# Optimization experiments

Hardware: AMD Instinct MI355X
Metric: run time of the kernel (lower is better)

## Reference

```python
import jax, jax.numpy as jnp
import numpy as np

DN = ('NCHW', 'OIHW', 'NCHW')
NUM_DOMAINS = 4


def conv2d(x, w, pad, groups=1):
    return jax.lax.conv_general_dilated(x, w, (1, 1), pad, dimension_numbers=DN,
                                        feature_group_count=groups)


def batchnorm2d(x, w, b, eps=1e-3):
    m = x.mean(axis=(0, 2, 3), keepdims=True)
    v = x.var(axis=(0, 2, 3), keepdims=True)
    return (x - m) / jnp.sqrt(v + eps) * w[None, :, None, None] + b[None, :, None, None]


def avgpool_w(x, k):
    B, C, H, W = x.shape
    Wo = W // k
    return x[..., :Wo * k].reshape(B, C, H, Wo, k).mean(axis=-1)


def mink(u, v):
    # Minkowski inner product <u,v>_L = -u0*v0 + <us,vs>
    return -u[..., 0] * v[..., 0] + (u[..., 1:] * v[..., 1:]).sum(-1)


def lorentz_elu(x):
    s = jax.nn.elu(x[..., 1:])
    t = jnp.sqrt(1.0 + (s * s).sum(-1, keepdims=True))
    return jnp.concatenate([t, s], -1)


def lorentz_avgpool_w(x, k):
    # (B,H,W,C) Lorentz points; window mean then Lorentz centroid projection
    B, H, W, C = x.shape
    Wo = W // k
    s = x[:, :, :Wo * k].reshape(B, H, Wo, k, C).mean(axis=3)
    d = jnp.sqrt(jnp.clip(jnp.abs(mink(s, s)), 1e-8, None))[..., None]
    return s / d


def lorentz_dbn(x, domains, beta, gamma, eps=1e-5):
    # Domain-specific Riemannian batch norm on the Lorentz manifold (k=1),
    # scalar dispersion (Frechet-mean centroid + geodesic variance per domain).
    B, H, W, C = x.shape
    pts = x.reshape(B, H * W, C)
    npts = float(H * W)
    s = jax.ops.segment_sum(pts.sum(axis=1), domains, num_segments=NUM_DOMAINS)  # (D,C)
    cnt = jax.ops.segment_sum(jnp.full((B,), npts, x.dtype), domains, num_segments=NUM_DOMAINS)
    cnt = jnp.maximum(cnt, 1.0)
    s = s / cnt[:, None]
    mu = s / jnp.sqrt(jnp.clip(jnp.abs(mink(s, s)), 1e-8, None))[:, None]  # (D,C) centroids
    mu_b = mu[domains][:, None, :]                                         # (B,1,C)
    ip = mink(mu_b, pts)                                                   # (B,HW)
    dist = jnp.arccosh(jnp.clip(-ip, 1.0 + 1e-7, None))
    u = pts + ip[..., None] * mu_b
    un = jnp.sqrt(jnp.clip(mink(u, u), 1e-8, None))
    v = dist[..., None] * u / un[..., None]                                # log_mu(x)
    var = jax.ops.segment_sum((dist ** 2).sum(axis=1), domains, num_segments=NUM_DOMAINS) / cnt
    o = jnp.zeros((C,), x.dtype).at[0].set(1.0)
    # parallel transport mu -> origin
    v = v + (-v[..., :1]) / (1.0 + mu_b[..., :1]) * (mu_b + o)
    # rescale by gamma / sqrt(var)
    v = v * (gamma / jnp.sqrt(var[domains] + eps))[:, None, None]
    # parallel transport origin -> beta, then expmap at beta
    v = v + (mink(beta, v) / (1.0 + beta[0]))[..., None] * (o + beta)
    vn = jnp.sqrt(jnp.clip(mink(v, v), 1e-8, None))[..., None]
    y = jnp.cosh(vn) * beta + jnp.sinh(vn) * v / vn
    return y.reshape(B, H, W, C)


def setup_inputs() -> dict:
    key = jax.random.key(0)
    ks = jax.random.split(key, 12)
    B = 128
    d = {}
    d['x'] = jax.random.normal(ks[0], (B, 32, 1024), jnp.float32)
    d['domains'] = jax.random.randint(ks[1], (B,), 0, NUM_DOMAINS, jnp.int32)
    d['conv1_w'] = 0.1 * jax.random.normal(ks[2], (16, 1, 1, 32), jnp.float32)
    d['bn1_w'] = jnp.ones((16,), jnp.float32)
    d['bn1_b'] = jnp.zeros((16,), jnp.float32)
    d['dw_w'] = 0.1 * jax.random.normal(ks[3], (32, 1, 32, 1), jnp.float32)
    d['bn2_w'] = jnp.ones((32,), jnp.float32)
    d['bn2_b'] = jnp.zeros((32,), jnp.float32)
    d['ec1_w'] = 0.1 * jax.random.normal(ks[4], (32, 1, 1, 16), jnp.float32)
    d['b2c1_w'] = 0.1 * jax.random.normal(ks[5], (32, 1, 1, 16), jnp.float32)
    d['b2c2_w'] = 0.1 * jax.random.normal(ks[6], (32, 32, 1, 1), jnp.float32)
    d['bn3_w'] = jnp.ones((32,), jnp.float32)
    d['bn3_b'] = jnp.zeros((32,), jnp.float32)
    d['lc1_w'] = 0.2 * jax.random.normal(ks[7], (33, 33), jnp.float32)
    d['bn_beta'] = jnp.zeros((33,), jnp.float32).at[0].set(1.0)
    d['bn_gamma'] = jnp.ones((1,), jnp.float32)
    d['mlr_a'] = 0.1 * jax.random.normal(ks[8], (1,), jnp.float32)
    d['mlr_z'] = 0.1 * jax.random.normal(ks[9], (1, 512), jnp.float32)
    return d


def reference(x, domains, conv1_w, bn1_w, bn1_b, dw_w, bn2_w, bn2_b, ec1_w,
              b2c1_w, b2c2_w, bn3_w, bn3_b, lc1_w, bn_beta, bn_gamma, mlr_a, mlr_z):
    h = x[:, None]                                       # (B,1,32,1024)
    # block1: temporal conv + BN + depthwise spatial conv + BN + ELU + pool
    h = conv2d(h, conv1_w, ((0, 0), (16, 16)))           # (B,16,32,1025)
    h = batchnorm2d(h, bn1_w, bn1_b)
    h = conv2d(h, dw_w, ((0, 0), (0, 0)), groups=16)     # (B,32,1,1025)
    h = batchnorm2d(h, bn2_w, bn2_b)
    h = jax.nn.elu(h)
    h = avgpool_w(h, 4)                                  # (B,32,1,256)
    # ec1 + block2
    h = conv2d(h, ec1_w, ((0, 0), (8, 8)), groups=32)    # (B,32,1,257)
    h = conv2d(h, b2c1_w, ((0, 0), (8, 8)), groups=32)   # (B,32,1,258)
    h = conv2d(h, b2c2_w, ((0, 0), (0, 0)))              # (B,32,1,258)
    h = batchnorm2d(h, bn3_w, bn3_b)
    h = jax.nn.elu(h)
    h = avgpool_w(h, 4)                                  # (B,32,1,64)
    # to Lorentz: permute, L2-normalize, pad time, projx (time = sqrt(1+|s|^2))
    h = jnp.transpose(h, (0, 2, 3, 1))                   # (B,1,64,32)
    h = h / jnp.clip(jnp.linalg.norm(h, axis=-1, keepdims=True), 1e-12, None)
    t = jnp.sqrt(1.0 + (h * h).sum(-1, keepdims=True))
    h = jnp.concatenate([t, h], -1)                      # (B,1,64,33)
    # LorentzConv2d kernel 1 == Lorentz fully-connected: linear then recompute time
    y = jnp.einsum('bhwc,oc->bhwo', h, lc1_w)
    ys = y[..., 1:]
    yt = jnp.sqrt(1.0 + (ys * ys).sum(-1, keepdims=True))
    h = jnp.concatenate([yt, ys], -1)                    # (B,1,64,33)
    h = lorentz_dbn(h, domains, bn_beta, bn_gamma)
    h = lorentz_elu(h)
    h = lorentz_avgpool_w(h, 4)                          # (B,1,16,33)
    # lorentz_flatten: concat spaces, recompute time -> (B, 16*32+1)
    B = h.shape[0]
    fs = h[..., 1:].reshape(B, -1)
    ft = jnp.sqrt(1.0 + (fs * fs).sum(-1, keepdims=True))
    features = jnp.concatenate([ft, fs], -1)             # (B,513)
    # Lorentz MLR (k=1)
    norm_z = jnp.linalg.norm(mlr_z, axis=-1)             # (1,)
    w_t = jnp.sinh(mlr_a) * norm_z
    bet = jnp.sqrt(jnp.clip(-w_t ** 2 + (jnp.cosh(mlr_a) * norm_z) ** 2, 1e-8, None))
    alpha = -w_t * features[:, :1] + jnp.cosh(mlr_a) * (features[:, 1:] @ mlr_z.T)
    dd = jnp.abs(jnp.arcsinh(alpha / bet))
    logits = jnp.sign(alpha) * bet * dd                  # (B,1)
    return logits.squeeze(-1), features
```

## Files before the change

### kernel.cpp

```cpp
#include <hip/hip_runtime.h>
#include <math.h>

#define Bn 128
#define Hh 32
#define Wx 1024
#define WP 1056

#define N1f 4198400.0f
#define N2f 131200.0f
#define N3f 33024.0f

#define OFF_C      0
#define OFF_S      32
#define OFF_EH     33
#define OFF_ET     48
#define OFF_G      64
#define OFF_G2     544
#define OFF_A1     1024
#define OFF_B1     1040
#define OFF_S1_2   1056
#define OFF_S2_2   1088
#define OFF_S1_3   1120
#define OFF_S2_3   1152
#define OFF_SEG    1184
#define OFF_CNT    1316
#define OFF_MU     1320
#define OFF_DSQ    1452
#define ZERO_N     1456
#define OFF_DWOUT  2048
#define OFF_E2     (2048 + 4194304)
#define OFF_C3     OFF_DWOUT
#define OFF_PTS    (OFF_C3 + 1056768)
#define OFF_VO     (OFF_PTS + 270336)

__device__ __forceinline__ float eluf(float x) { return x > 0.f ? x : expm1f(x); }

__global__ __launch_bounds__(256, 1) void k_corr(const float* __restrict__ x,
                                                 float* __restrict__ ws) {
    __shared__ float xs[1060];
    __shared__ float cacc[32];
    __shared__ float gacc[480];
    __shared__ float g2acc[480];
    __shared__ float eacc[30];
    int tid = threadIdx.x;
    for (int i = tid; i < 480; i += 256) { gacc[i] = 0.f; g2acc[i] = 0.f; }
    if (tid < 32) cacc[tid] = 0.f;
    if (tid < 30) eacc[tid] = 0.f;
    for (int i = 1024 + tid; i < 1060; i += 256) xs[i] = 0.f;
    float acc[32];
#pragma unroll
    for (int d = 0; d < 32; d++) acc[d] = 0.f;
    float sp = 0.f;
    int r0 = blockIdx.x * 16;
    for (int rr = 0; rr < 16; rr++) {
        __syncthreads();
        const float4* xr = (const float4*)(x + (r0 + rr) * Wx);
        ((float4*)xs)[tid] = xr[tid];
        __syncthreads();
        float v[36];
#pragma unroll
        for (int q = 0; q < 9; q++) {
            float4 t4 = ((const float4*)xs)[tid + q];
            v[4 * q] = t4.x; v[4 * q + 1] = t4.y; v[4 * q + 2] = t4.z; v[4 * q + 3] = t4.w;
        }
#pragma unroll
        for (int i = 0; i < 4; i++) {
            sp += v[i];
#pragma unroll
            for (int d = 0; d < 32; d++) acc[d] += v[i] * v[i + d];
        }
        if (tid < 240) {
#pragma unroll
            for (int q = 0; q < 2; q++) {
                int idx = tid * 2 + q;
                int d = idx / 15, j = idx - d * 15;
                gacc[idx]  += xs[j] * xs[j + d];
                g2acc[idx] += xs[1009 + j] * xs[1009 + j + d];
            }
        } else if (tid < 270) {
            int j = tid - 240;
            eacc[j] += (j < 15) ? xs[j] : xs[1009 + (j - 15)];
        }
    }
    int lane = tid & 63;
#pragma unroll
    for (int d = 0; d < 32; d++) {
        float vv = acc[d];
#pragma unroll
        for (int off = 32; off > 0; off >>= 1) vv += __shfl_down(vv, off);
        if (lane == 0) atomicAdd(&cacc[d], vv);
    }
    {
        float vv = sp;
#pragma unroll
        for (int off = 32; off > 0; off >>= 1) vv += __shfl_down(vv, off);
        if (lane == 0) atomicAdd(&ws[OFF_S], vv);
    }
    __syncthreads();
    if (tid < 32) atomicAdd(&ws[OFF_C + tid], cacc[tid]);
    for (int i = tid; i < 480; i += 256) {
        atomicAdd(&ws[OFF_G + i], gacc[i]);
        atomicAdd(&ws[OFF_G2 + i], g2acc[i]);
    }
    if (tid < 30) atomicAdd(&ws[OFF_EH + tid], eacc[tid]);
}

__global__ __launch_bounds__(512) void k_fold(const float* __restrict__ w1,
                                              const float* __restrict__ bn1w,
                                              const float* __restrict__ bn1b,
                                              float* __restrict__ ws) {
    __shared__ float PH[32][16];
    __shared__ float PT[32][16];
    __shared__ float Ts[32];
    __shared__ float w1s[512];
    __shared__ float sumsq[16];
    __shared__ float meanv[16];
    int tid = threadIdx.x;
    w1s[tid] = w1[tid];
    if (tid < 16) sumsq[tid] = 0.f;
    if (tid < 32) {
        int d = tid;
        float s = 0.f;
        for (int j = 0; j < 15; j++) { s += ws[OFF_G + d * 15 + j]; PH[d][j] = s; }
        float s2 = 0.f;
        for (int j = 14; j >= 0; j--) { s2 += ws[OFF_G2 + d * 15 + j]; PT[d][j] = s2; }
    } else if (tid >= 64 && tid < 96) {
        int k = tid - 64;
        float t = ws[OFF_S];
        for (int j = 0; j <= k - 17; j++) t -= ws[OFF_EH + j];
        if (k <= 14) for (int j = k; j < 15; j++) t -= ws[OFF_ET + j];
        Ts[k] = t;
    }
    __syncthreads();
    int c = tid >> 5, d = tid & 31;
    float Cd = ws[OFF_C + d];
    float part = 0.f;
    for (int k = 0; k + d < 32; k++) {
        float head = (k >= 17) ? PH[d][k - 17] : 0.f;
        float tail = (k <= 14) ? PT[d][k] : 0.f;
        float R = Cd - head - tail;
        part += w1s[c * 32 + k] * w1s[c * 32 + k + d] * R;
    }
    if (d > 0) part *= 2.f;
    atomicAdd(&sumsq[c], part);
    if (d == 0) {
        float mp = 0.f;
        for (int k = 0; k < 32; k++) mp += w1s[c * 32 + k] * Ts[k];
        meanv[c] = mp / N1f;
    }
    __syncthreads();
    if (tid < 16) {
        float mean = meanv[tid];
        float var = fmaxf(sumsq[tid] / N1f - mean * mean, 0.f);
        float a = bn1w[tid] / sqrtf(var + 1e-3f);
        ws[OFF_A1 + tid] = a;
        ws[OFF_B1 + tid] = bn1b[tid] - mean * a;
    }
}

__global__ __launch_bounds__(256) void k_dw(const float* __restrict__ x,
                                            const float* __restrict__ w1,
                                            const float* __restrict__ dww,
                                            float* __restrict__ ws) {
    __shared__ float dws[256];
    __shared__ float w1s[128];
    __shared__ float Dv[8];
    __shared__ float a1s[4], b1s[4];
    __shared__ float Ys[8 * WP];
    __shared__ float st[16];
    int tid = threadIdx.x;
    int b = blockIdx.x;
    int ocb = blockIdx.y * 8;
    int g0 = ocb >> 1;
    dws[tid] = dww[ocb * 32 + tid];
    if (tid < 128) w1s[tid] = w1[g0 * 32 + tid];
    if (tid < 16) st[tid] = 0.f;
    if (tid < 4) { a1s[tid] = ws[OFF_A1 + g0 + tid]; b1s[tid] = ws[OFF_B1 + g0 + tid]; }
    __syncthreads();
    if (tid < 8) {
        float d = 0.f;
        for (int h = 0; h < 32; h++) d += dws[tid * 32 + h];
        Dv[tid] = d;
    }
    for (int p = tid; p < WP; p += 256) {
        float acc[8];
#pragma unroll
        for (int j = 0; j < 8; j++) acc[j] = 0.f;
        bool inr = (p >= 16 && p < 16 + Wx);
        const float* xb = x + b * (Hh * Wx) + (p - 16);
        for (int h = 0; h < Hh; h++) {
            float xv = inr ? xb[h * Wx] : 0.f;
#pragma unroll
            for (int j = 0; j < 8; j++) acc[j] += xv * dws[j * 32 + h];
        }
#pragma unroll
        for (int j = 0; j < 8; j++) Ys[j * WP + p] = acc[j];
    }
    __syncthreads();
    float* dwout = ws + OFF_DWOUT;
    int lane = tid & 63;
    int wt = tid * 4;
    for (int j = 0; j < 8; j++) {
        int gl = j >> 1;
        float a = a1s[gl], bb = b1s[gl] * Dv[j];
        float wr[32];
#pragma unroll
        for (int k = 0; k < 32; k++) wr[k] = w1s[gl * 32 + k];
        float y[36];
        const float4* yp = (const float4*)(Ys + j * WP + wt);
#pragma unroll
        for (int q = 0; q < 9; q++) {
            float4 t4 = yp[q];
            y[4 * q] = t4.x; y[4 * q + 1] = t4.y; y[4 * q + 2] = t4.z; y[4 * q + 3] = t4.w;
        }
        float ls1 = 0.f, ls2 = 0.f;
        float outv[4];
#pragma unroll
        for (int m = 0; m < 4; m++) {
            float s = 0.f;
#pragma unroll
            for (int k = 0; k < 32; k++) s += wr[k] * y[m + k];
            float val = a * s + bb;
            outv[m] = val;
            ls1 += val; ls2 += val * val;
        }
        *((float4*)(dwout + (b * 32 + ocb + j) * 1024 + wt)) =
            make_float4(outv[0], outv[1], outv[2], outv[3]);
        if (tid == 0) {
            float s = 0.f;
#pragma unroll
            for (int k = 0; k < 32; k++) s += wr[k] * Ys[j * WP + 1024 + k];
            float val = a * s + bb;
            ls1 += val; ls2 += val * val;
        }
#pragma unroll
        for (int off = 32; off > 0; off >>= 1) {
            ls1 += __shfl_down(ls1, off);
            ls2 += __shfl_down(ls2, off);
        }
        if (lane == 0) { atomicAdd(&st[j], ls1); atomicAdd(&st[8 + j], ls2); }
    }
    __syncthreads();
    if (tid < 8) atomicAdd(&ws[OFF_S1_2 + ocb + tid], st[tid]);
    else if (tid < 16) atomicAdd(&ws[OFF_S2_2 + ocb + tid - 8], st[tid]);
}

__global__ __launch_bounds__(64) void k_pe(const float* __restrict__ ec1w,
                                           const float* __restrict__ bc1w,
                                           const float* __restrict__ bn2w,
                                           const float* __restrict__ bn2b,
                                           float* __restrict__ ws) {
    __shared__ float ins[272];
    __shared__ float e1p[288];
    int b = blockIdx.x, c = blockIdx.y;
    int t = threadIdx.x;
    if (t < 8) { ins[t] = 0.f; ins[264 + t] = 0.f; e1p[t] = 0.f; }
    if (t < 23) e1p[265 + t] = 0.f;
    float mean = ws[OFF_S1_2 + c] / N2f;
    float var = fmaxf(ws[OFF_S2_2 + c] / N2f - mean * mean, 0.f);
    float a = bn2w[c] / sqrtf(var + 1e-3f);
    float bb = bn2b[c] - mean * a;
    const float4* dr = (const float4*)(ws + OFF_DWOUT + (b * 32 + c) * 1024);
#pragma unroll
    for (int q = 0; q < 4; q++) {
        float4 v4 = dr[q * 64 + t];
        ins[8 + q * 64 + t] = 0.25f * (eluf(a * v4.x + bb) + eluf(a * v4.y + bb) +
                                       eluf(a * v4.z + bb) + eluf(a * v4.w + bb));
    }
    __syncthreads();
    float ek[16], bk[16];
#pragma unroll
    for (int k = 0; k < 16; k++) { ek[k] = ec1w[c * 16 + k]; bk[k] = bc1w[c * 16 + k]; }
    for (int w = t; w < 257; w += 64) {
        float s = 0.f;
#pragma unroll
        for (int k = 0; k < 16; k++) s += ins[w + k] * ek[k];
        e1p[8 + w] = s;
    }
    __syncthreads();
    float* e2r = ws + OFF_E2 + (b * 32 + c) * 258;
    for (int w = t; w < 258; w += 64) {
        float s = 0.f;
#pragma unroll
        for (int k = 0; k < 16; k++) s += e1p[w + k] * bk[k];
        e2r[w] = s;
    }
}

__global__ __launch_bounds__(256) void k_sep2(const float* __restrict__ bc2w,
                                              float* __restrict__ ws) {
    __shared__ float es[32 * 129];
    __shared__ float bs[1056];
    int b = blockIdx.x;
    int wb = blockIdx.y * 129;
    int t = threadIdx.x;
    for (int i = t; i < 1024; i += 256) { int o = i >> 5, cc = i & 31; bs[o * 33 + cc] = bc2w[i]; }
    const float* e2b = ws + OFF_E2 + b * 8256;
    for (int i = t; i < 4128; i += 256) {
        int cc = i / 129, wl = i - cc * 129;
        es[i] = e2b[cc * 258 + wb + wl];
    }
    __syncthreads();
    int o = t >> 3, w0 = t & 7;
    float wr[32];
#pragma unroll
    for (int cc = 0; cc < 32; cc++) wr[cc] = bs[o * 33 + cc];
    float s1 = 0.f, s2 = 0.f;
    float* c3r = ws + OFF_C3 + (b * 32 + o) * 258 + wb;
    for (int wl = w0; wl < 129; wl += 8) {
        float s = 0.f;
#pragma unroll
        for (int cc = 0; cc < 32; cc++) s += es[cc * 129 + wl] * wr[cc];
        c3r[wl] = s;
        s1 += s; s2 += s * s;
    }
    s1 += __shfl_down(s1, 4, 8); s1 += __shfl_down(s1, 2, 8); s1 += __shfl_down(s1, 1, 8);
    s2 += __shfl_down(s2, 4, 8); s2 += __shfl_down(s2, 2, 8); s2 += __shfl_down(s2, 1, 8);
    if (w0 == 0) {
        atomicAdd(&ws[OFF_S1_3 + o], s1);
        atomicAdd(&ws[OFF_S2_3 + o], s2);
    }
}

__global__ __launch_bounds__(256, 1) void k_head(const float* __restrict__ bn3w,
                                                 const float* __restrict__ bn3b,
                                                 const float* __restrict__ lc1w,
                                                 const int* __restrict__ domains,
                                                 float* __restrict__ ws) {
    __shared__ float q[2048];
    __shared__ float lc1s[1089];
    __shared__ float psum[33];
    __shared__ float ssyp[4][64];
    __shared__ float a3s[32], b3s[32];
    int tid = threadIdx.x;
    int b = blockIdx.x;
    if (tid < 32) {
        float mean = ws[OFF_S1_3 + tid] / N3f;
        float var = fmaxf(ws[OFF_S2_3 + tid] / N3f - mean * mean, 0.f);
        float a = bn3w[tid] / sqrtf(var + 1e-3f);
        a3s[tid] = a;
        b3s[tid] = bn3b[tid] - mean * a;
    }
    for (int i = tid; i < 1089; i += 256) lc1s[i] = lc1w[i];
    __syncthreads();
    const float* c3 = ws + OFF_C3 + b * 8256;
    for (int idx = tid; idx < 2048; idx += 256) {
        int c = idx >> 6, wp = idx & 63;
        float a = a3s[c], bb = b3s[c];
        float acc = 0.f;
#pragma unroll
        for (int j = 0; j < 4; j++) {
            float e = a * c3[c * 258 + wp * 4 + j] + bb;
            acc += eluf(e);
        }
        q[idx] = 0.25f * acc;
    }
    __syncthreads();
    int w = tid & 63, sub = tid >> 6;
    float qv[32];
    float ssq = 0.f;
#pragma unroll
    for (int c = 0; c < 32; c++) { qv[c] = q[c * 64 + w]; ssq += qv[c] * qv[c]; }
    float inv = 1.f / fmaxf(sqrtf(ssq), 1e-12f);
    float ss2 = 0.f;
#pragma unroll
    for (int c = 0; c < 32; c++) { qv[c] *= inv; ss2 += qv[c] * qv[c]; }
    float t = sqrtf(1.f + ss2);
    int o0 = 1 + sub * 8;
    float p[8];
    float ssy_part = 0.f;
#pragma unroll
    for (int i = 0; i < 8; i++) {
        int o = o0 + i;
        float s = lc1s[o * 33] * t;
#pragma unroll
        for (int c = 0; c < 32; c++) s += lc1s[o * 33 + 1 + c] * qv[c];
        p[i] = s;
        ssy_part += s * s;
    }
    ssyp[sub][w] = ssy_part;
    float* pr = ws + OFF_PTS + (b * 64 + w) * 33;
#pragma unroll
    for (int i = 0; i < 8; i++) pr[o0 + i] = p[i];
    __syncthreads();
    float yt = 0.f;
    if (sub == 0) {
        float ssy = ssyp[0][w] + ssyp[1][w] + ssyp[2][w] + ssyp[3][w];
        yt = sqrtf(1.f + ssy);
        pr[0] = yt;
    }
#pragma unroll
    for (int i = 0; i < 8; i++) {
        float vv = p[i];
#pragma unroll
        for (int off = 32; off > 0; off >>= 1) vv += __shfl_down(vv, off);
        if (w == 0) psum[o0 + i] = vv;
    }
    {
        float vv = yt;
#pragma unroll
        for (int off = 32; off > 0; off >>= 1) vv += __shfl_down(vv, off);
        if (w == 0 && sub == 0) psum[0] = vv;
    }
    __syncthreads();
    int dom = domains[b];
    if (tid < 33) atomicAdd(&ws[OFF_SEG + dom * 33 + tid], psum[tid]);
    if (tid == 64) atomicAdd(&ws[OFF_CNT + dom], 64.f);
}

__global__ void k_mu(float* __restrict__ ws) {
    int d = threadIdx.x;
    if (d < 4) {
        float cnt = fmaxf(ws[OFF_CNT + d], 1.f);
        float sv[33];
        float s0 = ws[OFF_SEG + d * 33] / cnt;
        sv[0] = s0;
        float sum = 0.f;
        for (int c = 1; c < 33; c++) {
            sv[c] = ws[OFF_SEG + d * 33 + c] / cnt;
            sum += sv[c] * sv[c];
        }
        float mk = -s0 * s0 + sum;
        float dn = sqrtf(fmaxf(fabsf(mk), 1e-8f));
        for (int c = 0; c < 33; c++) ws[OFF_MU + d * 33 + c] = sv[c] / dn;
    }
}

__global__ __launch_bounds__(64, 1) void k_tangent(const int* __restrict__ domains,
                                                   float* __restrict__ ws) {
    int b = blockIdx.x;
    int w = threadIdx.x;
    int dom = domains[b];
    const float* mu = ws + OFF_MU + dom * 33;
    const float* pr = ws + OFF_PTS + (b * 64 + w) * 33;
    float m[33], p[33];
#pragma unroll
    for (int c = 0; c < 33; c++) { m[c] = mu[c]; p[c] = pr[c]; }
    float ip = -m[0] * p[0];
#pragma unroll
    for (int c = 1; c < 33; c++) ip += m[c] * p[c];
    float z = fmaxf(-ip, 1.f + 1e-7f);
    float dist = acoshf(z);
    float u[33];
#pragma unroll
    for (int c = 0; c < 33; c++) u[c] = p[c] + ip * m[c];
    float mk = -u[0] * u[0];
#pragma unroll
    for (int c = 1; c < 33; c++) mk += u[c] * u[c];
    float un = sqrtf(fmaxf(mk, 1e-8f));
    float r = dist / un;
    float v0 = r * u[0];
    float coef = -v0 / (1.f + m[0]);
    float* vo = ws + OFF_VO + (b * 64 + w) * 33;
    vo[0] = v0 + coef * (m[0] + 1.f);
#pragma unroll
    for (int c = 1; c < 33; c++) vo[c] = r * u[c] + coef * m[c];
    float dsq = dist * dist;
#pragma unroll
    for (int off = 32; off > 0; off >>= 1) dsq += __shfl_down(dsq, off);
    if (w == 0) atomicAdd(&ws[OFF_DSQ + dom], dsq);
}

__global__ __launch_bounds__(64, 1) void k_final(const int* __restrict__ domains,
                                                 const float* __restrict__ beta,
                                                 const float* __restrict__ gamma,
                                                 const float* __restrict__ mlr_a,
                                                 const float* __restrict__ mlr_z,
                                                 float* __restrict__ ws,
                                                 float* __restrict__ out) {
    __shared__ float he[64 * 33];
    __shared__ float hp[16 * 33];
    int b = blockIdx.x;
    int w = threadIdx.x;
    int dom = domains[b];
    float cnt = fmaxf(ws[OFF_CNT + dom], 1.f);
    float var = ws[OFF_DSQ + dom] / cnt;
    float sc = gamma[0] / sqrtf(var + 1e-5f);
    float bt[33];
#pragma unroll
    for (int c = 0; c < 33; c++) bt[c] = beta[c];
    const float* vo = ws + OFF_VO + (b * 64 + w) * 33;
    float v[33];
#pragma unroll
    for (int c = 0; c < 33; c++) v[c] = vo[c] * sc;
    float mb = -bt[0] * v[0];
#pragma unroll
    for (int c = 1; c < 33; c++) mb += bt[c] * v[c];
    float coef = mb / (1.f + bt[0]);
    v[0] += coef * (1.f + bt[0]);
#pragma unroll
    for (int c = 1; c < 33; c++) v[c] += coef * bt[c];
    float mk = -v[0] * v[0];
#pragma unroll
    for (int c = 1; c < 33; c++) mk += v[c] * v[c];
    float vn = sqrtf(fmaxf(mk, 1e-8f));
    float ch = coshf(vn), sh = sinhf(vn) / vn;
    float ss = 0.f;
#pragma unroll
    for (int c = 1; c < 33; c++) {
        float y = ch * bt[c] + sh * v[c];
        float s = eluf(y);
        he[w * 33 + c] = s;
        ss += s * s;
    }
    he[w * 33] = sqrtf(1.f + ss);
    __syncthreads();
    if (w < 16) {
        float tmp[33];
        float mk2;
        {
            float a0 = 0.25f * (he[(4 * w) * 33] + he[(4 * w + 1) * 33] +
                                he[(4 * w + 2) * 33] + he[(4 * w + 3) * 33]);
            tmp[0] = a0;
            mk2 = -a0 * a0;
        }
#pragma unroll
        for (int c = 1; c < 33; c++) {
            float a = 0.25f * (he[(4 * w) * 33 + c] + he[(4 * w + 1) * 33 + c] +
                               he[(4 * w + 2) * 33 + c] + he[(4 * w + 3) * 33 + c]);
            tmp[c] = a;
            mk2 += a * a;
        }
        float dd = sqrtf(fmaxf(fabsf(mk2), 1e-8f));
#pragma unroll
        for (int c = 0; c < 33; c++) hp[w * 33 + c] = tmp[c] / dd;
    }
    __syncthreads();
    float ssq = 0.f, sdz = 0.f, zz = 0.f;
    for (int j = w; j < 512; j += 64) {
        float val = hp[(j >> 5) * 33 + 1 + (j & 31)];
        float zv = mlr_z[j];
        ssq += val * val;
        sdz += val * zv;
        zz += zv * zv;
        out[128 + b * 513 + 1 + j] = val;
    }
#pragma unroll
    for (int off = 32; off > 0; off >>= 1) {
        ssq += __shfl_down(ssq, off);
        sdz += __shfl_down(sdz, off);
        zz += __shfl_down(zz, off);
    }
    if (w == 0) {
        float nz = sqrtf(zz);
        float a = mlr_a[0];
        float cha = coshf(a);
        float wt = sinhf(a) * nz;
        float cn = cha * nz;
        float bet = sqrtf(fmaxf(cn * cn - wt * wt, 1e-8f));
        float ft = sqrtf(1.f + ssq);
        float alpha = -wt * ft + cha * sdz;
        out[128 + b * 513] = ft;
        out[b] = bet * asinhf(alpha / bet);
    }
}

extern "C" void kernel_launch(void* const* d_in, const int* in_sizes, int n_in,
                              void* d_out, int out_size, void* d_ws, size_t ws_size,
                              hipStream_t stream) {
    const float* x       = (const float*)d_in[0];
    const int*   domains = (const int*)d_in[1];
    const float* conv1_w = (const float*)d_in[2];
    const float* bn1_w   = (const float*)d_in[3];
    const float* bn1_b   = (const float*)d_in[4];
    const float* dw_w    = (const float*)d_in[5];
    const float* bn2_w   = (const float*)d_in[6];
    const float* bn2_b   = (const float*)d_in[7];
    const float* ec1_w   = (const float*)d_in[8];
    const float* b2c1_w  = (const float*)d_in[9];
    const float* b2c2_w  = (const float*)d_in[10];
    const float* bn3_w   = (const float*)d_in[11];
    const float* bn3_b   = (const float*)d_in[12];
    const float* lc1_w   = (const float*)d_in[13];
    const float* bn_beta = (const float*)d_in[14];
    const float* bn_gamma= (const float*)d_in[15];
    const float* mlr_a   = (const float*)d_in[16];
    const float* mlr_z   = (const float*)d_in[17];
    float* out = (float*)d_out;
    float* ws  = (float*)d_ws;

    hipMemsetAsync(ws, 0, ZERO_N * sizeof(float), stream);
    k_corr<<<256, 256, 0, stream>>>(x, ws);
    k_fold<<<1, 512, 0, stream>>>(conv1_w, bn1_w, bn1_b, ws);
    k_dw<<<dim3(128, 4), 256, 0, stream>>>(x, conv1_w, dw_w, ws);
    k_pe<<<dim3(128, 32), 64, 0, stream>>>(ec1_w, b2c1_w, bn2_w, bn2_b, ws);
    k_sep2<<<dim3(128, 2), 256, 0, stream>>>(b2c2_w, ws);
    k_head<<<Bn, 256, 0, stream>>>(bn3_w, bn3_b, lc1_w, domains, ws);
    k_mu<<<1, 64, 0, stream>>>(ws);
    k_tangent<<<Bn, 64, 0, stream>>>(domains, ws);
    k_final<<<Bn, 64, 0, stream>>>(domains, bn_beta, bn_gamma, mlr_a, mlr_z, ws, out);
}
```

Before: 245.0 us.

## Split edge stats kernel, spread corr and depthwise work over more blocks

Moves the per-row edge Gram and edge-sum statistics out of k_corr into a separate k_edge kernel. k_corr now runs 4 rows per block over 1024 blocks with double-buffered rows. Its per-block correlation partials go to a workspace array instead of global atomics, and k_fold reduces them. k_dw is split along width into 4 z-blocks, which shrinks shared memory and writes per-block BN partials that k_pe reduces. k_mu is folded into k_tangent, which recomputes the domain centroid itself. The aim is more parallelism on the heavy early kernels and fewer global atomics and launches, at the cost of an extra launch, redundant centroid work and extra partial-sum traffic.

```diff
diff --git a/kernel.cpp b/kernel.cpp
--- a/kernel.cpp
+++ b/kernel.cpp
@@ -4,63 +4,98 @@
 #define Bn 128
 #define Hh 32
 #define Wx 1024
-#define WP 1056
 
 #define N1f 4198400.0f
 #define N2f 131200.0f
 #define N3f 33024.0f
 
-#define OFF_C      0
-#define OFF_S      32
 #define OFF_EH     33
 #define OFF_ET     48
 #define OFF_G      64
 #define OFF_G2     544
 #define OFF_A1     1024
 #define OFF_B1     1040
-#define OFF_S1_2   1056
-#define OFF_S2_2   1088
-#define OFF_S1_3   1120
-#define OFF_S2_3   1152
-#define OFF_SEG    1184
-#define OFF_CNT    1316
-#define OFF_MU     1320
-#define OFF_DSQ    1452
-#define ZERO_N     1456
-#define OFF_DWOUT  2048
-#define OFF_E2     (2048 + 4194304)
+#define OFF_S1_3   1056
+#define OFF_S2_3   1088
+#define OFF_SEG    1120
+#define OFF_CNT    1252
+#define OFF_DSQ    1256
+#define ZERO_N     1280
+#define OFF_PC     2048
+#define OFF_PS     34816
+#define OFF_PD1    35840
+#define OFF_PD2    52224
+#define OFF_DWOUT  68608
+#define OFF_E2     (68608 + 4194304)
 #define OFF_C3     OFF_DWOUT
 #define OFF_PTS    (OFF_C3 + 1056768)
 #define OFF_VO     (OFF_PTS + 270336)
 
 __device__ __forceinline__ float eluf(float x) { return x > 0.f ? x : expm1f(x); }
 
+__global__ __launch_bounds__(256) void k_edge(const float* __restrict__ x,
+                                              float* __restrict__ ws) {
+    __shared__ float hd[64 * 48];
+    __shared__ float tl[64 * 48];
+    int tid = threadIdx.x;
+    int r0 = blockIdx.x * 64;
+    for (int i = tid; i < 64 * 32; i += 256) {
+        int r = i >> 5, c = i & 31;
+        tl[r * 48 + 16 + c] = 0.f;
+    }
+#pragma unroll
+    for (int it = 0; it < 4; it++) {
+        int idx = tid + it * 256;
+        int r = idx >> 4, q = idx & 15;
+        const float4* base = (const float4*)(x + (r0 + r) * Wx);
+        if (q < 12) ((float4*)(hd + r * 48))[q] = base[q];
+        else        ((float4*)(tl + r * 48))[q - 12] = base[252 + (q - 12)];
+    }
+    __syncthreads();
+    for (int p = tid; p < 990; p += 256) {
+        float acc = 0.f;
+        if (p < 480) {
+            int d = p / 15, j = p - d * 15;
+            for (int r = 0; r < 64; r++) acc += hd[r * 48 + j] * hd[r * 48 + j + d];
+            atomicAdd(&ws[OFF_G + p], acc);
+        } else if (p < 960) {
+            int p2 = p - 480;
+            int d = p2 / 15, j = p2 - d * 15;
+            for (int r = 0; r < 64; r++) acc += tl[r * 48 + 1 + j] * tl[r * 48 + 1 + j + d];
+            atomicAdd(&ws[OFF_G2 + p2], acc);
+        } else {
+            int j = p - 960;
+            if (j < 15) { for (int r = 0; r < 64; r++) acc += hd[r * 48 + j]; }
+            else        { for (int r = 0; r < 64; r++) acc += tl[r * 48 + 1 + (j - 15)]; }
+            atomicAdd(&ws[OFF_EH + j], acc);
+        }
+    }
+}
+
 __global__ __launch_bounds__(256, 1) void k_corr(const float* __restrict__ x,
                                                  float* __restrict__ ws) {
-    __shared__ float xs[1060];
+    __shared__ float xs[2][1060];
     __shared__ float cacc[32];
-    __shared__ float gacc[480];
-    __shared__ float g2acc[480];
-    __shared__ float eacc[30];
+    __shared__ float sacc;
     int tid = threadIdx.x;
-    for (int i = tid; i < 480; i += 256) { gacc[i] = 0.f; g2acc[i] = 0.f; }
     if (tid < 32) cacc[tid] = 0.f;
-    if (tid < 30) eacc[tid] = 0.f;
-    for (int i = 1024 + tid; i < 1060; i += 256) xs[i] = 0.f;
+    if (tid == 32) sacc = 0.f;
+    for (int i = 1024 + tid; i < 1060; i += 256) { xs[0][i] = 0.f; xs[1][i] = 0.f; }
     float acc[32];
 #pragma unroll
     for (int d = 0; d < 32; d++) acc[d] = 0.f;
     float sp = 0.f;
-    int r0 = blockIdx.x * 16;
-    for (int rr = 0; rr < 16; rr++) {
-        __syncthreads();
-        const float4* xr = (const float4*)(x + (r0 + rr) * Wx);
-        ((float4*)xs)[tid] = xr[tid];
-        __syncthreads();
+    int r0 = blockIdx.x * 4;
+    ((float4*)xs[0])[tid] = ((const float4*)(x + r0 * Wx))[tid];
+    __syncthreads();
+    for (int rr = 0; rr < 4; rr++) {
+        float4 nxt;
+        if (rr < 3) nxt = ((const float4*)(x + (r0 + rr + 1) * Wx))[tid];
+        const float* bq = xs[rr & 1];
         float v[36];
 #pragma unroll
         for (int q = 0; q < 9; q++) {
-            float4 t4 = ((const float4*)xs)[tid + q];
+            float4 t4 = ((const float4*)bq)[tid + q];
             v[4 * q] = t4.x; v[4 * q + 1] = t4.y; v[4 * q + 2] = t4.z; v[4 * q + 3] = t4.w;
         }
 #pragma unroll
@@ -69,18 +104,8 @@
 #pragma unroll
             for (int d = 0; d < 32; d++) acc[d] += v[i] * v[i + d];
         }
-        if (tid < 240) {
-#pragma unroll
-            for (int q = 0; q < 2; q++) {
-                int idx = tid * 2 + q;
-                int d = idx / 15, j = idx - d * 15;
-                gacc[idx]  += xs[j] * xs[j + d];
-                g2acc[idx] += xs[1009 + j] * xs[1009 + j + d];
-            }
-        } else if (tid < 270) {
-            int j = tid - 240;
-            eacc[j] += (j < 15) ? xs[j] : xs[1009 + (j - 15)];
-        }
+        if (rr < 3) ((float4*)xs[(rr + 1) & 1])[tid] = nxt;
+        __syncthreads();
     }
     int lane = tid & 63;
 #pragma unroll
@@ -94,15 +119,11 @@
         float vv = sp;
 #pragma unroll
         for (int off = 32; off > 0; off >>= 1) vv += __shfl_down(vv, off);
-        if (lane == 0) atomicAdd(&ws[OFF_S], vv);
-    }
-    __syncthreads();
-    if (tid < 32) atomicAdd(&ws[OFF_C + tid], cacc[tid]);
-    for (int i = tid; i < 480; i += 256) {
-        atomicAdd(&ws[OFF_G + i], gacc[i]);
-        atomicAdd(&ws[OFF_G2 + i], g2acc[i]);
-    }
-    if (tid < 30) atomicAdd(&ws[OFF_EH + tid], eacc[tid]);
+        if (lane == 0) atomicAdd(&sacc, vv);
+    }
+    __syncthreads();
+    if (tid < 32) ws[OFF_PC + tid * 1024 + blockIdx.x] = cacc[tid];
+    if (tid == 32) ws[OFF_PS + blockIdx.x] = sacc;
 }
 
 __global__ __launch_bounds__(512) void k_fold(const float* __restrict__ w1,
@@ -115,25 +136,49 @@
     __shared__ float w1s[512];
     __shared__ float sumsq[16];
     __shared__ float meanv[16];
+    __shared__ float Cs[32];
+    __shared__ float sS[16];
     int tid = threadIdx.x;
     w1s[tid] = w1[tid];
     if (tid < 16) sumsq[tid] = 0.f;
+    {
+        int d = tid >> 4, i = tid & 15;
+        const float4* pc = (const float4*)(ws + OFF_PC + d * 1024 + i * 64);
+        float s = 0.f;
+#pragma unroll
+        for (int k = 0; k < 16; k++) { float4 t4 = pc[k]; s += t4.x + t4.y + t4.z + t4.w; }
+        s += __shfl_down(s, 8); s += __shfl_down(s, 4);
+        s += __shfl_down(s, 2); s += __shfl_down(s, 1);
+        if (i == 0) Cs[d] = s;
+    }
+    __syncthreads();
     if (tid < 32) {
         int d = tid;
         float s = 0.f;
         for (int j = 0; j < 15; j++) { s += ws[OFF_G + d * 15 + j]; PH[d][j] = s; }
         float s2 = 0.f;
         for (int j = 14; j >= 0; j--) { s2 += ws[OFF_G2 + d * 15 + j]; PT[d][j] = s2; }
-    } else if (tid >= 64 && tid < 96) {
+    } else if (tid < 48) {
+        int i = tid - 32;
+        const float4* ps = (const float4*)(ws + OFF_PS + i * 64);
+        float s = 0.f;
+#pragma unroll
+        for (int k = 0; k < 16; k++) { float4 t4 = ps[k]; s += t4.x + t4.y + t4.z + t4.w; }
+        sS[i] = s;
+    }
+    __syncthreads();
+    if (tid >= 64 && tid < 96) {
         int k = tid - 64;
-        float t = ws[OFF_S];
+        float S = 0.f;
+        for (int j = 0; j < 16; j++) S += sS[j];
+        float t = S;
         for (int j = 0; j <= k - 17; j++) t -= ws[OFF_EH + j];
         if (k <= 14) for (int j = k; j < 15; j++) t -= ws[OFF_ET + j];
         Ts[k] = t;
     }
     __syncthreads();
     int c = tid >> 5, d = tid & 31;
-    float Cd = ws[OFF_C + d];
+    float Cd = Cs[d];
     float part = 0.f;
     for (int k = 0; k + d < 32; k++) {
         float head = (k >= 17) ? PH[d][k - 17] : 0.f;
@@ -158,19 +203,21 @@
     }
 }
 
-__global__ __launch_bounds__(256) void k_dw(const float* __restrict__ x,
-                                            const float* __restrict__ w1,
-                                            const float* __restrict__ dww,
-                                            float* __restrict__ ws) {
+__global__ __launch_bounds__(256, 1) void k_dw(const float* __restrict__ x,
+                                               const float* __restrict__ w1,
+                                               const float* __restrict__ dww,
+                                               float* __restrict__ ws) {
     __shared__ float dws[256];
     __shared__ float w1s[128];
     __shared__ float Dv[8];
     __shared__ float a1s[4], b1s[4];
-    __shared__ float Ys[8 * WP];
+    __shared__ float Ys[8 * 296];
     __shared__ float st[16];
     int tid = threadIdx.x;
     int b = blockIdx.x;
     int ocb = blockIdx.y * 8;
+    int z = blockIdx.z;
+    int wt0 = z * 256;
     int g0 = ocb >> 1;
     dws[tid] = dww[ocb * 32 + tid];
     if (tid < 128) w1s[tid] = w1[g0 * 32 + tid];
@@ -182,67 +229,54 @@
         for (int h = 0; h < 32; h++) d += dws[tid * 32 + h];
         Dv[tid] = d;
     }
-    for (int p = tid; p < WP; p += 256) {
+    for (int p = wt0 + tid; p < wt0 + 288; p += 256) {
         float acc[8];
 #pragma unroll
         for (int j = 0; j < 8; j++) acc[j] = 0.f;
         bool inr = (p >= 16 && p < 16 + Wx);
         const float* xb = x + b * (Hh * Wx) + (p - 16);
         for (int h = 0; h < Hh; h++) {
-            float xv = inr ? xb[h * Wx] : 0.f;
+            float xv = inr ? xb[h << 10] : 0.f;
 #pragma unroll
             for (int j = 0; j < 8; j++) acc[j] += xv * dws[j * 32 + h];
         }
 #pragma unroll
-        for (int j = 0; j < 8; j++) Ys[j * WP + p] = acc[j];
-    }
-    __syncthreads();
-    float* dwout = ws + OFF_DWOUT;
+        for (int j = 0; j < 8; j++) Ys[j * 296 + (p - wt0)] = acc[j];
+    }
+    __syncthreads();
+    int w = wt0 + tid;
     int lane = tid & 63;
-    int wt = tid * 4;
-    for (int j = 0; j < 8; j++) {
-        int gl = j >> 1;
-        float a = a1s[gl], bb = b1s[gl] * Dv[j];
+    for (int jp = 0; jp < 4; jp++) {
         float wr[32];
 #pragma unroll
-        for (int k = 0; k < 32; k++) wr[k] = w1s[gl * 32 + k];
-        float y[36];
-        const float4* yp = (const float4*)(Ys + j * WP + wt);
-#pragma unroll
-        for (int q = 0; q < 9; q++) {
-            float4 t4 = yp[q];
-            y[4 * q] = t4.x; y[4 * q + 1] = t4.y; y[4 * q + 2] = t4.z; y[4 * q + 3] = t4.w;
-        }
-        float ls1 = 0.f, ls2 = 0.f;
-        float outv[4];
-#pragma unroll
-        for (int m = 0; m < 4; m++) {
+        for (int k = 0; k < 32; k++) wr[k] = w1s[jp * 32 + k];
+#pragma unroll
+        for (int jj = 0; jj < 2; jj++) {
+            int j = jp * 2 + jj;
             float s = 0.f;
-#pragma unroll
-            for (int k = 0; k < 32; k++) s += wr[k] * y[m + k];
-            float val = a * s + bb;
-            outv[m] = val;
-            ls1 += val; ls2 += val * val;
-        }
-        *((float4*)(dwout + (b * 32 + ocb + j) * 1024 + wt)) =
-            make_float4(outv[0], outv[1], outv[2], outv[3]);
-        if (tid == 0) {
-            float s = 0.f;
-#pragma unroll
-            for (int k = 0; k < 32; k++) s += wr[k] * Ys[j * WP + 1024 + k];
-            float val = a * s + bb;
-            ls1 += val; ls2 += val * val;
-        }
-#pragma unroll
-        for (int off = 32; off > 0; off >>= 1) {
-            ls1 += __shfl_down(ls1, off);
-            ls2 += __shfl_down(ls2, off);
-        }
-        if (lane == 0) { atomicAdd(&st[j], ls1); atomicAdd(&st[8 + j], ls2); }
-    }
-    __syncthreads();
-    if (tid < 8) atomicAdd(&ws[OFF_S1_2 + ocb + tid], st[tid]);
-    else if (tid < 16) atomicAdd(&ws[OFF_S2_2 + ocb + tid - 8], st[tid]);
+#pragma unroll 8
+            for (int k = 0; k < 32; k++) s += wr[k] * Ys[j * 296 + tid + k];
+            float val = a1s[jp] * s + b1s[jp] * Dv[j];
+            ws[OFF_DWOUT + (b * 32 + ocb + j) * 1024 + w] = val;
+            float ls1 = val, ls2 = val * val;
+            if (z == 3 && tid == 0) {
+                float s2 = 0.f;
+#pragma unroll
+                for (int k = 0; k < 32; k++) s2 += wr[k] * Ys[j * 296 + 256 + k];
+                float v2 = a1s[jp] * s2 + b1s[jp] * Dv[j];
+                ls1 += v2; ls2 += v2 * v2;
+            }
+#pragma unroll
+            for (int off = 32; off > 0; off >>= 1) {
+                ls1 += __shfl_down(ls1, off);
+                ls2 += __shfl_down(ls2, off);
+            }
+            if (lane == 0) { atomicAdd(&st[j], ls1); atomicAdd(&st[8 + j], ls2); }
+        }
+    }
+    __syncthreads();
+    if (tid < 8)       ws[OFF_PD1 + (ocb + tid) * 512 + z * 128 + b] = st[tid];
+    else if (tid < 16) ws[OFF_PD2 + (ocb + tid - 8) * 512 + z * 128 + b] = st[tid];
 }
 
 __global__ __launch_bounds__(64) void k_pe(const float* __restrict__ ec1w,
@@ -256,8 +290,18 @@
     int t = threadIdx.x;
     if (t < 8) { ins[t] = 0.f; ins[264 + t] = 0.f; e1p[t] = 0.f; }
     if (t < 23) e1p[265 + t] = 0.f;
-    float mean = ws[OFF_S1_2 + c] / N2f;
-    float var = fmaxf(ws[OFF_S2_2 + c] / N2f - mean * mean, 0.f);
+    const float4* p1 = (const float4*)(ws + OFF_PD1 + c * 512);
+    const float4* p2 = (const float4*)(ws + OFF_PD2 + c * 512);
+    float4 a0 = p1[t * 2], a1 = p1[t * 2 + 1], c0 = p2[t * 2], c1 = p2[t * 2 + 1];
+    float s1 = a0.x + a0.y + a0.z + a0.w + a1.x + a1.y + a1.z + a1.w;
+    float s2 = c0.x + c0.y + c0.z + c0.w + c1.x + c1.y + c1.z + c1.w;
+#pragma unroll
+    for (int off = 32; off > 0; off >>= 1) {
+        s1 += __shfl_xor(s1, off);
+        s2 += __shfl_xor(s2, off);
+    }
+    float mean = s1 / N2f;
+    float var = fmaxf(s2 / N2f - mean * mean, 0.f);
     float a = bn2w[c] / sqrtf(var + 1e-3f);
     float bb = bn2b[c] - mean * a;
     const float4* dr = (const float4*)(ws + OFF_DWOUT + (b * 32 + c) * 1024);
@@ -408,34 +452,29 @@
     if (tid == 64) atomicAdd(&ws[OFF_CNT + dom], 64.f);
 }
 
-__global__ void k_mu(float* __restrict__ ws) {
-    int d = threadIdx.x;
-    if (d < 4) {
-        float cnt = fmaxf(ws[OFF_CNT + d], 1.f);
-        float sv[33];
-        float s0 = ws[OFF_SEG + d * 33] / cnt;
-        sv[0] = s0;
-        float sum = 0.f;
-        for (int c = 1; c < 33; c++) {
-            sv[c] = ws[OFF_SEG + d * 33 + c] / cnt;
-            sum += sv[c] * sv[c];
-        }
-        float mk = -s0 * s0 + sum;
-        float dn = sqrtf(fmaxf(fabsf(mk), 1e-8f));
-        for (int c = 0; c < 33; c++) ws[OFF_MU + d * 33 + c] = sv[c] / dn;
-    }
-}
-
 __global__ __launch_bounds__(64, 1) void k_tangent(const int* __restrict__ domains,
                                                    float* __restrict__ ws) {
     int b = blockIdx.x;
     int w = threadIdx.x;
     int dom = domains[b];
-    const float* mu = ws + OFF_MU + dom * 33;
+    float cnt = fmaxf(ws[OFF_CNT + dom], 1.f);
+    float m[33];
+    float s0 = ws[OFF_SEG + dom * 33] / cnt;
+    m[0] = s0;
+    float msum = 0.f;
+#pragma unroll
+    for (int c = 1; c < 33; c++) {
+        m[c] = ws[OFF_SEG + dom * 33 + c] / cnt;
+        msum += m[c] * m[c];
+    }
+    float mkm = -s0 * s0 + msum;
+    float dn = 1.f / sqrtf(fmaxf(fabsf(mkm), 1e-8f));
+#pragma unroll
+    for (int c = 0; c < 33; c++) m[c] *= dn;
     const float* pr = ws + OFF_PTS + (b * 64 + w) * 33;
-    float m[33], p[33];
-#pragma unroll
-    for (int c = 0; c < 33; c++) { m[c] = mu[c]; p[c] = pr[c]; }
+    float p[33];
+#pragma unroll
+    for (int c = 0; c < 33; c++) p[c] = pr[c];
     float ip = -m[0] * p[0];
 #pragma unroll
     for (int c = 1; c < 33; c++) ip += m[c] * p[c];
@@ -580,13 +619,13 @@
     float* ws  = (float*)d_ws;
 
     hipMemsetAsync(ws, 0, ZERO_N * sizeof(float), stream);
-    k_corr<<<256, 256, 0, stream>>>(x, ws);
+    k_edge<<<64, 256, 0, stream>>>(x, ws);
+    k_corr<<<1024, 256, 0, stream>>>(x, ws);
     k_fold<<<1, 512, 0, stream>>>(conv1_w, bn1_w, bn1_b, ws);
-    k_dw<<<dim3(128, 4), 256, 0, stream>>>(x, conv1_w, dw_w, ws);
+    k_dw<<<dim3(128, 4, 4), 256, 0, stream>>>(x, conv1_w, dw_w, ws);
     k_pe<<<dim3(128, 32), 64, 0, stream>>>(ec1_w, b2c1_w, bn2_w, bn2_b, ws);
     k_sep2<<<dim3(128, 2), 256, 0, stream>>>(b2c2_w, ws);
     k_head<<<Bn, 256, 0, stream>>>(bn3_w, bn3_b, lc1_w, domains, ws);
-    k_mu<<<1, 64, 0, stream>>>(ws);
     k_tangent<<<Bn, 64, 0, stream>>>(domains, ws);
     k_final<<<Bn, 64, 0, stream>>>(domains, bn_beta, bn_gamma, mlr_a, mlr_z, ws, out);
 }
```

New measurement: 291.3 us. 18.9% more time.
